# Optimization experiments

Hardware: AMD Instinct MI355X
Metric: run time of the kernel (lower is better)

Reference implementation:

```python
import jax, jax.numpy as jnp
import numpy as np

N_AGENTS = 16      # args['num_agents']
BATCH = 8192       # args['n_rollout_threads'] -> number of independent graphs
OBS = 64           # cent_obs_shape[0] // n_nodes
HID = 128          # args['hidden_sizes'][0]
N_LAYERS = 2       # args['n_layers']
USE_RES = True     # args['use_res']


def _build_edges():
    # complete graph (no self loops) per graph, block-diagonal over BATCH graphs
    i, j = np.meshgrid(np.arange(N_AGENTS), np.arange(N_AGENTS), indexing='ij')
    m = i != j
    bs, bd = i[m], j[m]                      # [240]
    off = (np.arange(BATCH) * N_AGENTS)[:, None]
    src = (bs[None, :] + off).ravel().astype(np.int32)  # [BATCH*240]
    dst = (bd[None, :] + off).ravel().astype(np.int32)
    return src, dst


def setup_inputs() -> dict:
    key = jax.random.key(0)
    ks = jax.random.split(key, 5)
    N = BATCH * N_AGENTS
    src, dst = _build_edges()
    return {
        'cent_obs': jax.random.normal(ks[0], (N, OBS), jnp.float32),
        'w_emb': jax.random.normal(ks[1], (OBS, HID), jnp.float32) / np.sqrt(OBS).astype(np.float32),
        'b_emb': jnp.zeros((HID,), jnp.float32),
        'w_gcn': jax.random.normal(ks[2], (N_LAYERS, HID, HID), jnp.float32) / np.sqrt(HID).astype(np.float32),
        'b_gcn': jnp.zeros((N_LAYERS, HID), jnp.float32),
        'w_fc1': jax.random.normal(ks[3], (HID, 1), jnp.float32) / np.sqrt(HID).astype(np.float32),
        'b_fc1': jnp.zeros((1,), jnp.float32),
        'edge_src': jnp.asarray(src),
        'edge_dst': jnp.asarray(dst),
    }


def reference(cent_obs, w_emb, b_emb, w_gcn, b_gcn, w_fc1, b_fc1, edge_src, edge_dst):
    N = cent_obs.shape[0]
    # embedding_in
    x = cent_obs @ w_emb + b_emb                           # [N, HID]
    # GCNConv normalization with added self-loops (PyG default, sym norm)
    loop = jnp.arange(N, dtype=edge_src.dtype)
    src = jnp.concatenate([edge_src, loop])
    dst = jnp.concatenate([edge_dst, loop])
    deg = jax.ops.segment_sum(jnp.ones_like(dst, dtype=x.dtype), dst, num_segments=N)
    inv_sqrt = jax.lax.rsqrt(deg)
    norm = (inv_sqrt[src] * inv_sqrt[dst])[:, None]        # [E+N, 1]
    for l in range(N_LAYERS):
        h = x @ w_gcn[l]                                   # linear transform
        agg = jax.ops.segment_sum(h[src] * norm, dst, num_segments=N) + b_gcn[l]
        x = jnp.tanh(agg + x if USE_RES else agg)
    value = x @ w_fc1 + b_fc1                              # [N, 1]
    value = value.reshape(BATCH, -1)                       # [BATCH, n_nodes]
    return value.mean(axis=1).reshape(-1, 1)               # [BATCH, 1]
```

## Files before the change

### kernel.cpp

```cpp
#include <hip/hip_runtime.h>


#define N_GRAPHS 8192
#define BLOCK    256
#define NBLOCKS  (N_GRAPHS / 8)

typedef __attribute__((ext_vector_type(8)))  short short8;
typedef __attribute__((ext_vector_type(4)))  float floatx4;
typedef __attribute__((ext_vector_type(16))) float floatx16;

#define MFMA16(a, b, c) __builtin_amdgcn_mfma_f32_16x16x32_bf16((a), (b), (c), 0, 0, 0)
#define MFMA32(a, b, c) __builtin_amdgcn_mfma_f32_32x32x16_bf16((a), (b), (c), 0, 0, 0)

#define EMB_LO   1024
#define GCN_BASE 2048
#define GCN_LO   2048
#define N_FRAGS  10240

__device__ __forceinline__ unsigned fbits(float x) {
  union { float f; unsigned u; } v; v.f = x; return v.u;
}
__device__ __forceinline__ float bitsf(unsigned u) {
  union { float f; unsigned u; } v; v.u = u; return v.f;
}
__device__ __forceinline__ void bsplit(float x, short& hi, short& lo) {
  unsigned hb = fbits(x) & 0xFFFF0000u;
  hi = (short)(hb >> 16);
  lo = (short)(fbits(x - bitsf(hb)) >> 16);
}
__device__ __forceinline__ float fast_tanh(float z) {
  float e = __expf(2.0f * z);
  return 1.0f - 2.0f / (e + 1.0f);
}

__global__ __launch_bounds__(BLOCK) void gcn_prep(
    const float* __restrict__ w_emb, const float* __restrict__ w_gcn,
    short8* __restrict__ ws)
{
  int f = blockIdx.x * BLOCK + threadIdx.x;
  if (f >= 5120) return;
  const float* src;
  int hi_idx, lo_idx;
  if (f < 1024) {
    int ks = f >> 8, t = (f >> 6) & 3, L = f & 63;
    int k0 = ks * 16 + (L >> 5) * 8;
    int n  = t * 32 + (L & 31);
    src = w_emb + k0 * 128 + n;
    hi_idx = f; lo_idx = f + EMB_LO;
  } else {
    int f2 = f - 1024;
    int l = f2 >> 11, r = f2 & 2047;
    int kc = r >> 9, nt = (r >> 6) & 7, L = r & 63;
    int k0 = kc * 32 + (L >> 4) * 8;
    int n  = nt * 16 + (L & 15);
    src = w_gcn + l * 16384 + k0 * 128 + n;
    hi_idx = GCN_BASE + l * 4096 + r; lo_idx = hi_idx + GCN_LO;
  }
  short8 hi, lo;
  #pragma unroll
  for (int j = 0; j < 8; ++j) {
    short h, l_;
    bsplit(src[j * 128], h, l_);
    hi[j] = h; lo[j] = l_;
  }
  ws[hi_idx] = hi;
  ws[lo_idx] = lo;
}

__global__ __launch_bounds__(BLOCK, 4) void gcn_main(
    const float* __restrict__ obs,
    const float* __restrict__ b_emb,
    const float* __restrict__ b_gcn,
    const float* __restrict__ w_fc1,
    const float* __restrict__ b_fc1,
    const short8* __restrict__ tab,
    float* __restrict__ out)
{
  __shared__ float sM[8][129];
  __shared__ float sH[8][129];

  const int tid = threadIdx.x;
  const int w   = tid >> 6;
  const int L   = tid & 63;
  const int m32 = L & 31;
  const int kh  = L >> 5;
  const int c16 = L & 15;
  const int q   = L >> 4;
  const int G0  = blockIdx.x * 8;
  const int gw  = G0 + 2 * w;

  const float* op = obs + (gw * 16 + m32) * 64 + kh * 8;
  float4 ov[4][2];
  #pragma unroll
  for (int s = 0; s < 4; ++s) {
    ov[s][0] = *(const float4*)(op + s * 16);
    ov[s][1] = *(const float4*)(op + s * 16 + 4);
  }

  floatx16 x[4];
  #pragma unroll
  for (int t = 0; t < 4; ++t) {
    float b = b_emb[t * 32 + m32];
    #pragma unroll
    for (int r = 0; r < 16; ++r) x[t][r] = b;
  }
  #pragma unroll
  for (int s = 0; s < 4; ++s) {
    float tmp[8] = {ov[s][0].x, ov[s][0].y, ov[s][0].z, ov[s][0].w,
                    ov[s][1].x, ov[s][1].y, ov[s][1].z, ov[s][1].w};
    short8 ah, al;
    #pragma unroll
    for (int j = 0; j < 8; ++j) {
      short h, l_;
      bsplit(tmp[j], h, l_);
      ah[j] = h; al[j] = l_;
    }
    #pragma unroll
    for (int t = 0; t < 4; ++t) {
      int idx = (s * 4 + t) * 64 + L;
      short8 bh = tab[idx];
      short8 bl = tab[idx + EMB_LO];
      x[t] = MFMA32(ah, bh, x[t]);
      x[t] = MFMA32(al, bh, x[t]);
      x[t] = MFMA32(ah, bl, x[t]);
    }
  }

  #pragma unroll 1
  for (int l = 0; l < 2; ++l) {
    #pragma unroll
    for (int t = 0; t < 4; ++t) {
      float s0 = 0.f, s1 = 0.f;
      #pragma unroll
      for (int r = 0; r < 8; ++r) { s0 += x[t][r]; s1 += x[t][r + 8]; }
      s0 += __shfl_xor(s0, 32);
      s1 += __shfl_xor(s1, 32);
      if (L < 32) {
        sM[2 * w][t * 32 + L]     = s0 * 0.0625f;
        sM[2 * w + 1][t * 32 + L] = s1 * 0.0625f;
      }
    }
    __syncthreads();

    floatx4 h0 = {0.f, 0.f, 0.f, 0.f};
    floatx4 h1 = {0.f, 0.f, 0.f, 0.f};
    #pragma unroll
    for (int kc = 0; kc < 4; ++kc) {
      short8 ah, al;
      #pragma unroll
      for (int j = 0; j < 8; ++j) {
        int k = kc * 32 + q * 8 + j;
        float mv = sM[c16 & 7][k];
        if (c16 >= 8) mv = 0.f;
        short h, l_;
        bsplit(mv, h, l_);
        ah[j] = h; al[j] = l_;
      }
      int base = GCN_BASE + l * 4096 + kc * 8 * 64 + L;
      short8 bh0 = tab[base + (2 * w) * 64];
      short8 bl0 = tab[base + (2 * w) * 64 + GCN_LO];
      short8 bh1 = tab[base + (2 * w + 1) * 64];
      short8 bl1 = tab[base + (2 * w + 1) * 64 + GCN_LO];
      h0 = MFMA16(ah, bh0, h0); h0 = MFMA16(al, bh0, h0); h0 = MFMA16(ah, bl0, h0);
      h1 = MFMA16(ah, bh1, h1); h1 = MFMA16(al, bh1, h1); h1 = MFMA16(ah, bl1, h1);
    }
    if (q < 2) {
      #pragma unroll
      for (int r = 0; r < 4; ++r) {
        sH[q * 4 + r][(2 * w) * 16 + c16]     = h0[r];
        sH[q * 4 + r][(2 * w + 1) * 16 + c16] = h1[r];
      }
    }
    __syncthreads();

    #pragma unroll
    for (int t = 0; t < 4; ++t) {
      float b  = b_gcn[l * 128 + t * 32 + m32];
      float zA = sH[2 * w][t * 32 + m32] + b;
      float zB = sH[2 * w + 1][t * 32 + m32] + b;
      #pragma unroll
      for (int r = 0; r < 8; ++r) {
        x[t][r]     = fast_tanh(x[t][r] + zA);
        x[t][r + 8] = fast_tanh(x[t][r + 8] + zB);
      }
    }
  }

  float vA = 0.f, vB = 0.f;
  #pragma unroll
  for (int t = 0; t < 4; ++t) {
    float wf = w_fc1[t * 32 + m32];
    float sA = 0.f, sB = 0.f;
    #pragma unroll
    for (int r = 0; r < 8; ++r) { sA += x[t][r]; sB += x[t][r + 8]; }
    vA = fmaf(sA, wf, vA);
    vB = fmaf(sB, wf, vB);
  }
  #pragma unroll
  for (int d = 32; d >= 1; d >>= 1) {
    vA += __shfl_xor(vA, d);
    vB += __shfl_xor(vB, d);
  }
  if (L == 0) {
    float bf = b_fc1[0];
    out[gw]     = vA * 0.0625f + bf;
    out[gw + 1] = vB * 0.0625f + bf;
  }
}

extern "C" void kernel_launch(void* const* d_in, const int* in_sizes, int n_in,
                              void* d_out, int out_size, void* d_ws, size_t ws_size,
                              hipStream_t stream) {
  const float* obs    = (const float*)d_in[0];
  const float* w_emb  = (const float*)d_in[1];
  const float* b_emb  = (const float*)d_in[2];
  const float* w_gcn  = (const float*)d_in[3];
  const float* b_gcn  = (const float*)d_in[4];
  const float* w_fc1  = (const float*)d_in[5];
  const float* b_fc1  = (const float*)d_in[6];
  float* out = (float*)d_out;
  short8* tab = (short8*)d_ws;

  gcn_prep<<<20, BLOCK, 0, stream>>>(w_emb, w_gcn, tab);
  gcn_main<<<NBLOCKS, BLOCK, 0, stream>>>(obs, b_emb, b_gcn, w_fc1, b_fc1,
                                          tab, out);
}
```

Measured before the change: 122.6 us.

## Pre-split bf16 fragments into LDS and software-pipeline weight loads in GCN kernel

The GCN layer's mean vector is now split into bf16 hi/lo on write and stored as packed fragments in shared memory, so each MFMA operand comes from one vector LDS read instead of eight scalar reads plus per-element splitting. Weight fragments for the next k-chunk are prefetched before the current MFMAs run. The obs loads are double-buffered and packing uses byte-perm. The prep kernel now runs one thread per element for more parallelism. Side effects are extra LDS zero-init work and more live registers.

```diff
diff --git a/kernel.cpp b/kernel.cpp
--- a/kernel.cpp
+++ b/kernel.cpp
@@ -15,7 +15,8 @@
 #define EMB_LO   1024
 #define GCN_BASE 2048
 #define GCN_LO   2048
-#define N_FRAGS  10240
+
+union fragu { unsigned int u[4]; short8 s8; };
 
 __device__ __forceinline__ unsigned fbits(float x) {
   union { float f; unsigned u; } v; v.f = x; return v.u;
@@ -28,25 +29,49 @@
   hi = (short)(hb >> 16);
   lo = (short)(fbits(x - bitsf(hb)) >> 16);
 }
+__device__ __forceinline__ unsigned hpack(unsigned b_odd, unsigned b_even) {
+  return __builtin_amdgcn_perm(b_odd, b_even, 0x07060302u);
+}
+__device__ __forceinline__ void mk_frags(float4 a, float4 b, short8& hi, short8& lo) {
+  fragu H, L;
+  H.u[0] = hpack(fbits(a.y), fbits(a.x));
+  H.u[1] = hpack(fbits(a.w), fbits(a.z));
+  H.u[2] = hpack(fbits(b.y), fbits(b.x));
+  H.u[3] = hpack(fbits(b.w), fbits(b.z));
+  float l0 = a.x - bitsf(fbits(a.x) & 0xFFFF0000u);
+  float l1 = a.y - bitsf(fbits(a.y) & 0xFFFF0000u);
+  float l2 = a.z - bitsf(fbits(a.z) & 0xFFFF0000u);
+  float l3 = a.w - bitsf(fbits(a.w) & 0xFFFF0000u);
+  float l4 = b.x - bitsf(fbits(b.x) & 0xFFFF0000u);
+  float l5 = b.y - bitsf(fbits(b.y) & 0xFFFF0000u);
+  float l6 = b.z - bitsf(fbits(b.z) & 0xFFFF0000u);
+  float l7 = b.w - bitsf(fbits(b.w) & 0xFFFF0000u);
+  L.u[0] = hpack(fbits(l1), fbits(l0));
+  L.u[1] = hpack(fbits(l3), fbits(l2));
+  L.u[2] = hpack(fbits(l5), fbits(l4));
+  L.u[3] = hpack(fbits(l7), fbits(l6));
+  hi = H.s8; lo = L.s8;
+}
 __device__ __forceinline__ float fast_tanh(float z) {
   float e = __expf(2.0f * z);
-  return 1.0f - 2.0f / (e + 1.0f);
+  return 1.0f - __fdividef(2.0f, e + 1.0f);
 }
 
 __global__ __launch_bounds__(BLOCK) void gcn_prep(
     const float* __restrict__ w_emb, const float* __restrict__ w_gcn,
-    short8* __restrict__ ws)
+    unsigned short* __restrict__ wsS)
 {
-  int f = blockIdx.x * BLOCK + threadIdx.x;
-  if (f >= 5120) return;
+  int idx = blockIdx.x * BLOCK + threadIdx.x;
+  if (idx >= 40960) return;
+  int f = idx >> 3, j = idx & 7;
   const float* src;
-  int hi_idx, lo_idx;
+  int hi_f, lo_f;
   if (f < 1024) {
     int ks = f >> 8, t = (f >> 6) & 3, L = f & 63;
     int k0 = ks * 16 + (L >> 5) * 8;
     int n  = t * 32 + (L & 31);
     src = w_emb + k0 * 128 + n;
-    hi_idx = f; lo_idx = f + EMB_LO;
+    hi_f = f; lo_f = f + EMB_LO;
   } else {
     int f2 = f - 1024;
     int l = f2 >> 11, r = f2 & 2047;
@@ -54,17 +79,12 @@
     int k0 = kc * 32 + (L >> 4) * 8;
     int n  = nt * 16 + (L & 15);
     src = w_gcn + l * 16384 + k0 * 128 + n;
-    hi_idx = GCN_BASE + l * 4096 + r; lo_idx = hi_idx + GCN_LO;
-  }
-  short8 hi, lo;
-  #pragma unroll
-  for (int j = 0; j < 8; ++j) {
-    short h, l_;
-    bsplit(src[j * 128], h, l_);
-    hi[j] = h; lo[j] = l_;
-  }
-  ws[hi_idx] = hi;
-  ws[lo_idx] = lo;
+    hi_f = GCN_BASE + l * 4096 + r; lo_f = hi_f + GCN_LO;
+  }
+  short h, l_;
+  bsplit(src[j * 128], h, l_);
+  wsS[hi_f * 8 + j] = (unsigned short)h;
+  wsS[lo_f * 8 + j] = (unsigned short)l_;
 }
 
 __global__ __launch_bounds__(BLOCK, 4) void gcn_main(
@@ -76,7 +96,7 @@
     const short8* __restrict__ tab,
     float* __restrict__ out)
 {
-  __shared__ float sM[8][129];
+  __shared__ short sA[2 * 4 * 16 * 40];
   __shared__ float sH[8][129];
 
   const int tid = threadIdx.x;
@@ -86,16 +106,25 @@
   const int kh  = L >> 5;
   const int c16 = L & 15;
   const int q   = L >> 4;
-  const int G0  = blockIdx.x * 8;
-  const int gw  = G0 + 2 * w;
+  const int gw  = blockIdx.x * 8 + 2 * w;
+
+  {
+    unsigned int* za = (unsigned int*)sA;
+    #pragma unroll
+    for (int jz = 0; jz < 5; ++jz) {
+      int i   = tid + 256 * jz;
+      int tb_ = i / 160;
+      int rm  = i - tb_ * 160;
+      int rr  = rm / 20, cw = rm - rr * 20;
+      za[tb_ * 320 + (rr + 8) * 20 + cw] = 0;
+    }
+  }
 
   const float* op = obs + (gw * 16 + m32) * 64 + kh * 8;
-  float4 ov[4][2];
-  #pragma unroll
-  for (int s = 0; s < 4; ++s) {
-    ov[s][0] = *(const float4*)(op + s * 16);
-    ov[s][1] = *(const float4*)(op + s * 16 + 4);
-  }
+  float4 oa0 = *(const float4*)(op);
+  float4 oa1 = *(const float4*)(op + 4);
+  float4 ob0 = *(const float4*)(op + 16);
+  float4 ob1 = *(const float4*)(op + 20);
 
   floatx16 x[4];
   #pragma unroll
@@ -104,16 +133,15 @@
     #pragma unroll
     for (int r = 0; r < 16; ++r) x[t][r] = b;
   }
+
   #pragma unroll
   for (int s = 0; s < 4; ++s) {
-    float tmp[8] = {ov[s][0].x, ov[s][0].y, ov[s][0].z, ov[s][0].w,
-                    ov[s][1].x, ov[s][1].y, ov[s][1].z, ov[s][1].w};
     short8 ah, al;
-    #pragma unroll
-    for (int j = 0; j < 8; ++j) {
-      short h, l_;
-      bsplit(tmp[j], h, l_);
-      ah[j] = h; al[j] = l_;
+    mk_frags(oa0, oa1, ah, al);
+    oa0 = ob0; oa1 = ob1;
+    if (s < 2) {
+      ob0 = *(const float4*)(op + (s + 2) * 16);
+      ob1 = *(const float4*)(op + (s + 2) * 16 + 4);
     }
     #pragma unroll
     for (int t = 0; t < 4; ++t) {
@@ -128,16 +156,31 @@
 
   #pragma unroll 1
   for (int l = 0; l < 2; ++l) {
+    const short8* t0 = tab + GCN_BASE + l * 4096 + (2 * w) * 64 + L;
+    const short8* t1 = t0 + 64;
+    short8 cbh0 = t0[0], cbh1 = t1[0];
+    short8 cbl0 = t0[GCN_LO], cbl1 = t1[GCN_LO];
+
     #pragma unroll
     for (int t = 0; t < 4; ++t) {
-      float s0 = 0.f, s1 = 0.f;
-      #pragma unroll
-      for (int r = 0; r < 8; ++r) { s0 += x[t][r]; s1 += x[t][r + 8]; }
+      float s0 = x[t][0], s1 = x[t][8];
+      #pragma unroll
+      for (int r = 1; r < 8; ++r) { s0 += x[t][r]; s1 += x[t][r + 8]; }
       s0 += __shfl_xor(s0, 32);
       s1 += __shfl_xor(s1, 32);
-      if (L < 32) {
-        sM[2 * w][t * 32 + L]     = s0 * 0.0625f;
-        sM[2 * w + 1][t * 32 + L] = s1 * 0.0625f;
+      s0 *= 0.0625f; s1 *= 0.0625f;
+      #pragma unroll
+      for (int rr = 0; rr < 2; ++rr) {
+        float v = rr ? s1 : s0;
+        unsigned hb = fbits(v) & 0xFFFF0000u;
+        unsigned vb = (kh == 0) ? hb : fbits(v - bitsf(hb));
+        unsigned nb = (unsigned)__shfl_xor((int)vb, 1);
+        unsigned pw = hpack(nb, vb);
+        if ((m32 & 1) == 0) {
+          int si = kh * 2560 + t * 640 + (2 * w + rr) * 40
+                 + (m32 >> 3) * 8 + (m32 & 7);
+          *(unsigned int*)&sA[si] = pw;
+        }
       }
     }
     __syncthreads();
@@ -146,23 +189,19 @@
     floatx4 h1 = {0.f, 0.f, 0.f, 0.f};
     #pragma unroll
     for (int kc = 0; kc < 4; ++kc) {
-      short8 ah, al;
-      #pragma unroll
-      for (int j = 0; j < 8; ++j) {
-        int k = kc * 32 + q * 8 + j;
-        float mv = sM[c16 & 7][k];
-        if (c16 >= 8) mv = 0.f;
-        short h, l_;
-        bsplit(mv, h, l_);
-        ah[j] = h; al[j] = l_;
-      }
-      int base = GCN_BASE + l * 4096 + kc * 8 * 64 + L;
-      short8 bh0 = tab[base + (2 * w) * 64];
-      short8 bl0 = tab[base + (2 * w) * 64 + GCN_LO];
-      short8 bh1 = tab[base + (2 * w + 1) * 64];
-      short8 bl1 = tab[base + (2 * w + 1) * 64 + GCN_LO];
-      h0 = MFMA16(ah, bh0, h0); h0 = MFMA16(al, bh0, h0); h0 = MFMA16(ah, bl0, h0);
-      h1 = MFMA16(ah, bh1, h1); h1 = MFMA16(al, bh1, h1); h1 = MFMA16(ah, bl1, h1);
+      short8 ah = *(const short8*)&sA[kc * 640 + c16 * 40 + q * 8];
+      short8 al = *(const short8*)&sA[2560 + kc * 640 + c16 * 40 + q * 8];
+      short8 nbh0, nbh1, nbl0, nbl1;
+      if (kc < 3) {
+        nbh0 = t0[(kc + 1) * 512];
+        nbh1 = t1[(kc + 1) * 512];
+        nbl0 = t0[(kc + 1) * 512 + GCN_LO];
+        nbl1 = t1[(kc + 1) * 512 + GCN_LO];
+      }
+      h0 = MFMA16(ah, cbh0, h0); h1 = MFMA16(ah, cbh1, h1);
+      h0 = MFMA16(al, cbh0, h0); h1 = MFMA16(al, cbh1, h1);
+      h0 = MFMA16(ah, cbl0, h0); h1 = MFMA16(ah, cbl1, h1);
+      cbh0 = nbh0; cbh1 = nbh1; cbl0 = nbl0; cbl1 = nbl1;
     }
     if (q < 2) {
       #pragma unroll
@@ -190,11 +229,11 @@
   #pragma unroll
   for (int t = 0; t < 4; ++t) {
     float wf = w_fc1[t * 32 + m32];
-    float sA = 0.f, sB = 0.f;
-    #pragma unroll
-    for (int r = 0; r < 8; ++r) { sA += x[t][r]; sB += x[t][r + 8]; }
-    vA = fmaf(sA, wf, vA);
-    vB = fmaf(sB, wf, vB);
+    float sA_ = 0.f, sB_ = 0.f;
+    #pragma unroll
+    for (int r = 0; r < 8; ++r) { sA_ += x[t][r]; sB_ += x[t][r + 8]; }
+    vA = fmaf(sA_, wf, vA);
+    vB = fmaf(sB_, wf, vB);
   }
   #pragma unroll
   for (int d = 32; d >= 1; d >>= 1) {
@@ -219,9 +258,8 @@
   const float* w_fc1  = (const float*)d_in[5];
   const float* b_fc1  = (const float*)d_in[6];
   float* out = (float*)d_out;
-  short8* tab = (short8*)d_ws;
-
-  gcn_prep<<<20, BLOCK, 0, stream>>>(w_emb, w_gcn, tab);
+
+  gcn_prep<<<160, BLOCK, 0, stream>>>(w_emb, w_gcn, (unsigned short*)d_ws);
   gcn_main<<<NBLOCKS, BLOCK, 0, stream>>>(obs, b_emb, b_gcn, w_fc1, b_fc1,
-                                          tab, out);
-}
+                                          (const short8*)d_ws, out);
+}
```

New measurement: 119.7 us. 2.4% less time.
